# Optimization experiments

Measured on AMD Instinct MI355X. Metric: run time of the kernel, lower is better.

The kernel has to match this reference:

```python
import jax, jax.numpy as jnp
import numpy as np

N_HEAD = 8

def _l2norm(x, eps=1e-12):
    # F.normalize(p=2, dim=-1): x / max(||x||_2, eps)
    return x / jnp.maximum(jnp.linalg.norm(x, axis=-1, keepdims=True), eps)

def setup_inputs() -> dict:
    key = jax.random.key(0)
    ks = jax.random.split(key, 9)
    B, L, E = 2, 2048, 512
    s = 0.02
    return {
        "query": jax.random.normal(ks[0], (B, L, E), dtype=jnp.float32),
        "Wq": s * jax.random.normal(ks[1], (E, E), dtype=jnp.float32),
        "bq": jnp.zeros((E,), dtype=jnp.float32),
        "Wk": s * jax.random.normal(ks[2], (E, E), dtype=jnp.float32),
        "bk": jnp.zeros((E,), dtype=jnp.float32),
        "Wv": s * jax.random.normal(ks[3], (E, E), dtype=jnp.float32),
        "bv": jnp.zeros((E,), dtype=jnp.float32),
        "Wo": s * jax.random.normal(ks[4], (E, E), dtype=jnp.float32),
        "bo": jnp.zeros((E,), dtype=jnp.float32),
    }

def reference(query, Wq, bq, Wk, bk, Wv, bv, Wo, bo):
    B, L, E = query.shape
    H = N_HEAD
    hd = E // H
    # Faithful to torch: .view(tgt_len, bsz, E) is a RESHAPE, not a transpose.
    x = query.reshape(L, B, E)
    q = jax.nn.relu(x @ Wq.T + bq)
    k = jax.nn.relu(x @ Wk.T + bk)
    v = x @ Wv.T + bv
    q = _l2norm(q)
    k = _l2norm(k)
    # (L, B, E) -> (L, B*H, hd) -> (B*H, L, hd)
    q_ = q.reshape(L, B * H, hd).transpose(1, 0, 2)
    k_ = k.reshape(L, B * H, hd).transpose(1, 0, 2)
    v_ = v.reshape(L, B * H, hd).transpose(1, 0, 2)
    # Causal linear attention: cumulative outer-product of k,v then contract with q.
    kv = jnp.einsum('nld,nlm->nldm', k_, v_)      # [B*H, L, hd, hd]
    kv_cum = jnp.cumsum(kv, axis=1)
    out = jnp.einsum('nld,nldm->nlm', q_, kv_cum)  # [B*H, L, hd]
    out = out.transpose(1, 0, 2).reshape(L, B, E)
    out = out @ Wo.T + bo
    return out.reshape(B, L, E)
```

## Files before the change

### kernel.cpp

```cpp
#include <hip/hip_runtime.h>
#include <hip/hip_bf16.h>

typedef __attribute__((ext_vector_type(8))) short short8;
typedef __attribute__((ext_vector_type(4))) float f32x4;
using bf16 = __hip_bfloat16;

__device__ __forceinline__ unsigned short f2bf(float f) {
    unsigned u = __float_as_uint(f);
    u += 0x7fff + ((u >> 16) & 1);
    return (unsigned short)(u >> 16);
}
__device__ __forceinline__ float bf2f(unsigned short s) {
    return __uint_as_float(((unsigned)s) << 16);
}
__device__ __forceinline__ void gl_lds16(const unsigned short* g, unsigned short* l) {
    __builtin_amdgcn_global_load_lds(
        (const __attribute__((address_space(1))) unsigned int*)g,
        (__attribute__((address_space(3))) unsigned int*)l, 16, 0, 0);
}


__global__ __launch_bounds__(256) void pack_kernel(
    const float* __restrict__ X, const float* __restrict__ Wq, const float* __restrict__ Wk,
    const float* __restrict__ Wv, const float* __restrict__ Wo,
    bf16* __restrict__ Xp, bf16* __restrict__ Wqp, bf16* __restrict__ Wkp,
    bf16* __restrict__ Wvp, bf16* __restrict__ Wop, float* __restrict__ ssq)
{
    __shared__ __align__(16) unsigned short sm[4096];
    int id = blockIdx.x;
    int tid = threadIdx.x;
    if (id < 8) {
        int zi = id * 1024 + tid * 4;
        *(float4*)&ssq[zi] = make_float4(0.f, 0.f, 0.f, 0.f);
    }
    const float* src; unsigned short* dst; int g, sc;
    if (id < 512) { src = X; dst = (unsigned short*)Xp; g = id >> 3; sc = id & 7; }
    else {
        int t = id - 512; int wsel = t >> 6; int u = t & 63;
        g = u >> 3; sc = u & 7;
        src = (wsel == 0) ? Wq : ((wsel == 1) ? Wk : ((wsel == 2) ? Wv : Wo));
        dst = (unsigned short*)((wsel == 0) ? Wqp : ((wsel == 1) ? Wkp : ((wsel == 2) ? Wvp : Wop)));
    }
    int r = tid >> 2, kq = tid & 3;
    const float* sp = src + (size_t)(g * 64 + r) * 512 + sc * 64 + kq * 16;
    #pragma unroll
    for (int i = 0; i < 4; ++i) {
        float4 v = *(const float4*)(sp + i * 4);
        int kk = kq * 16 + i * 4;
        int sl = kk >> 3, el = kk & 7;
        ushort4 u4;
        u4.x = f2bf(v.x); u4.y = f2bf(v.y); u4.z = f2bf(v.z); u4.w = f2bf(v.w);
        *(ushort4*)&sm[(sl * 64 + r) * 8 + el] = u4;
    }
    __syncthreads();
    unsigned short* dp = dst + (size_t)g * 32768 + sc * 4096;
    *(uint4*)(dp + tid * 16)     = *(const uint4*)&sm[tid * 16];
    *(uint4*)(dp + tid * 16 + 8) = *(const uint4*)&sm[tid * 16 + 8];
}

__global__ __launch_bounds__(256) void qkv_gemm_kernel(
    const bf16* __restrict__ Xp,
    const bf16* __restrict__ W0p, const bf16* __restrict__ W1p, const bf16* __restrict__ W2p,
    const float* __restrict__ b0, const float* __restrict__ b1, const float* __restrict__ b2,
    bf16* __restrict__ O0, bf16* __restrict__ O1, bf16* __restrict__ O2,
    float* __restrict__ ssq)
{
    __shared__ __align__(16) unsigned short smem[32768];
    const unsigned short* Ag  = (const unsigned short*)Xp;
    const unsigned short* W0g = (const unsigned short*)W0p;
    const unsigned short* W1g = (const unsigned short*)W1p;
    const unsigned short* W2g = (const unsigned short*)W2p;
    int g = blockIdx.x, gy = blockIdx.y;
    int m0 = g * 64, n0 = gy * 64;
    int tid = threadIdx.x;
    int lane = tid & 63;
    int w = tid >> 6;
    int wm = (w >> 1) * 32;
    int wn = (w & 1) * 32;
    int fr = lane & 15, qf = lane >> 4;

    f32x4 zero4 = {0.f, 0.f, 0.f, 0.f};
    f32x4 acc[3][2][2];
    #pragma unroll
    for (int z = 0; z < 3; ++z)
        #pragma unroll
        for (int t = 0; t < 2; ++t)
            #pragma unroll
            for (int u = 0; u < 2; ++u) acc[z][t][u] = zero4;

#define QKV_STAGE(buf, it) do {                                                              \
        unsigned short* bb = smem + (buf) * 16384;                                           \
        int s0_ = (it) * 8 + w * 2;                                                          \
        gl_lds16(Ag  + ((size_t)(g  * 64 + s0_)     * 64 + lane) * 8, bb + (w * 2)     * 512);        \
        gl_lds16(Ag  + ((size_t)(g  * 64 + s0_ + 1) * 64 + lane) * 8, bb + (w * 2 + 1) * 512);        \
        gl_lds16(W0g + ((size_t)(gy * 64 + s0_)     * 64 + lane) * 8, bb + 4096  + (w * 2)     * 512); \
        gl_lds16(W0g + ((size_t)(gy * 64 + s0_ + 1) * 64 + lane) * 8, bb + 4096  + (w * 2 + 1) * 512); \
        gl_lds16(W1g + ((size_t)(gy * 64 + s0_)     * 64 + lane) * 8, bb + 8192  + (w * 2)     * 512); \
        gl_lds16(W1g + ((size_t)(gy * 64 + s0_ + 1) * 64 + lane) * 8, bb + 8192  + (w * 2 + 1) * 512); \
        gl_lds16(W2g + ((size_t)(gy * 64 + s0_)     * 64 + lane) * 8, bb + 12288 + (w * 2)     * 512); \
        gl_lds16(W2g + ((size_t)(gy * 64 + s0_ + 1) * 64 + lane) * 8, bb + 12288 + (w * 2 + 1) * 512); \
    } while (0)

    int cur = 0;
    QKV_STAGE(0, 0);
    __syncthreads();
    for (int it = 0; it < 8; ++it) {
        if (it < 7) QKV_STAGE(cur ^ 1, it + 1);
        const unsigned short* As = smem + cur * 16384;
        #pragma unroll
        for (int kk = 0; kk < 2; ++kk) {
            int ks = (kk * 4 + qf) * 64;
            short8 af[2];
            af[0] = *(const short8*)&As[(ks + wm + fr) * 8];
            af[1] = *(const short8*)&As[(ks + wm + 16 + fr) * 8];
            #pragma unroll
            for (int z = 0; z < 3; ++z) {
                const unsigned short* Bs = As + 4096 + z * 4096;
                short8 bf0 = *(const short8*)&Bs[(ks + wn + fr) * 8];
                short8 bf1 = *(const short8*)&Bs[(ks + wn + 16 + fr) * 8];
                acc[z][0][0] = __builtin_amdgcn_mfma_f32_16x16x32_bf16(af[0], bf0, acc[z][0][0], 0, 0, 0);
                acc[z][0][1] = __builtin_amdgcn_mfma_f32_16x16x32_bf16(af[0], bf1, acc[z][0][1], 0, 0, 0);
                acc[z][1][0] = __builtin_amdgcn_mfma_f32_16x16x32_bf16(af[1], bf0, acc[z][1][0], 0, 0, 0);
                acc[z][1][1] = __builtin_amdgcn_mfma_f32_16x16x32_bf16(af[1], bf1, acc[z][1][1], 0, 0, 0);
            }
        }
        __syncthreads();
        cur ^= 1;
    }
#undef QKV_STAGE

    int rb = qf * 4;
    #pragma unroll
    for (int z = 0; z < 3; ++z) {
        const float* bias = (z == 0) ? b0 : ((z == 1) ? b1 : b2);
        #pragma unroll
        for (int u = 0; u < 2; ++u) {
            float bv = bias[n0 + wn + u * 16 + fr];
            #pragma unroll
            for (int t = 0; t < 2; ++t)
                #pragma unroll
                for (int r = 0; r < 4; ++r) {
                    float v = acc[z][t][u][r] + bv;
                    if (z < 2) v = fmaxf(v, 0.f);
                    acc[z][t][u][r] = v;
                }
        }
    }
    #pragma unroll
    for (int z = 0; z < 2; ++z)
        #pragma unroll
        for (int t = 0; t < 2; ++t)
            #pragma unroll
            for (int r = 0; r < 4; ++r) {
                float s = acc[z][t][0][r] * acc[z][t][0][r] + acc[z][t][1][r] * acc[z][t][1][r];
                #pragma unroll
                for (int off = 1; off < 16; off <<= 1) s += __shfl_xor(s, off, 64);
                if (fr == 0) atomicAdd(&ssq[z * 4096 + m0 + wm + t * 16 + rb + r], s);
            }
    #pragma unroll
    for (int z = 0; z < 3; ++z)
        #pragma unroll
        for (int t = 0; t < 2; ++t)
            #pragma unroll
            for (int u = 0; u < 2; ++u)
                #pragma unroll
                for (int r = 0; r < 4; ++r)
                    smem[z * 4096 + (wm + t * 16 + rb + r) * 64 + wn + u * 16 + fr] = f2bf(acc[z][t][u][r]);
    __syncthreads();
    unsigned short* O0s = (unsigned short*)O0;
    unsigned short* O1s = (unsigned short*)O1;
    unsigned short* O2s = (unsigned short*)O2;
    #pragma unroll
    for (int rep = 0; rep < 6; ++rep) {
        int idx = rep * 256 + tid;
        int z = idx >> 9, rem = idx & 511;
        int row = rem >> 3, col8 = (rem & 7) * 8;
        unsigned short* Oz = (z == 0) ? O0s : ((z == 1) ? O1s : O2s);
        *(uint4*)(Oz + (size_t)(m0 + row) * 512 + n0 + col8) = *(const uint4*)&smem[z * 4096 + row * 64 + col8];
    }
}

__global__ __launch_bounds__(256) void chunk_kv_kernel(
    const bf16* __restrict__ Kb, const bf16* __restrict__ Vb,
    const float* __restrict__ ssq, bf16* __restrict__ ScT, bf16* __restrict__ Vt_g)
{
    int n = blockIdx.x >> 5, c = blockIdx.x & 31;
    int b = n >> 3, h = n & 7;
    __shared__ float Ks[64 * 64];
    __shared__ float Vs[64 * 64];
    const unsigned short* Kg = (const unsigned short*)Kb;
    const unsigned short* Vg = (const unsigned short*)Vb;
    int tid = threadIdx.x;
    int td = tid >> 4, tm = tid & 15;
    int d0 = td * 4, m0 = tm * 4;
    #pragma unroll
    for (int rep = 0; rep < 4; ++rep) {
        int idx = rep * 1024 + tid * 4;
        int j = idx >> 6, d = idx & 63;
        int grow = (c * 64 + j) * 2 + b;
        ushort4 ku = *(const ushort4*)&Kg[(size_t)grow * 512 + h * 64 + d];
        ushort4 vu = *(const ushort4*)&Vg[(size_t)grow * 512 + h * 64 + d];
        float rk = 1.f / fmaxf(sqrtf(ssq[4096 + grow]), 1e-12f);
        *(float4*)&Ks[j * 64 + d] = make_float4(bf2f(ku.x), bf2f(ku.y), bf2f(ku.z), bf2f(ku.w));
        *(float4*)&Vs[j * 64 + d] = make_float4(bf2f(vu.x) * rk, bf2f(vu.y) * rk,
                                                bf2f(vu.z) * rk, bf2f(vu.w) * rk);
    }
    __syncthreads();
    float acc[4][4] = {};
    for (int j = 0; j < 64; ++j) {
        float4 kv = *(const float4*)&Ks[j * 64 + d0];
        float4 vv = *(const float4*)&Vs[j * 64 + m0];
        acc[0][0] += kv.x*vv.x; acc[0][1] += kv.x*vv.y; acc[0][2] += kv.x*vv.z; acc[0][3] += kv.x*vv.w;
        acc[1][0] += kv.y*vv.x; acc[1][1] += kv.y*vv.y; acc[1][2] += kv.y*vv.z; acc[1][3] += kv.y*vv.w;
        acc[2][0] += kv.z*vv.x; acc[2][1] += kv.z*vv.y; acc[2][2] += kv.z*vv.z; acc[2][3] += kv.z*vv.w;
        acc[3][0] += kv.w*vv.x; acc[3][1] += kv.w*vv.y; acc[3][2] += kv.w*vv.z; acc[3][3] += kv.w*vv.w;
    }
    int vm = tid & 63, vj0 = (tid >> 6) * 16;
    unsigned short tmp[16];
    #pragma unroll
    for (int i = 0; i < 16; ++i) tmp[i] = f2bf(Vs[(vj0 + i) * 64 + vm]);
    size_t vtoff = (size_t)n * 131072 + (size_t)vm * 2048 + c * 64 + vj0;
    *(uint4*)((unsigned short*)Vt_g + vtoff)     = *(uint4*)&tmp[0];
    *(uint4*)((unsigned short*)Vt_g + vtoff + 8) = *(uint4*)&tmp[8];

    unsigned short* outp = (unsigned short*)ScT + (size_t)blockIdx.x * 4096;
    #pragma unroll
    for (int j2 = 0; j2 < 4; ++j2) {
        ushort4 o4;
        o4.x = f2bf(acc[0][j2]); o4.y = f2bf(acc[1][j2]);
        o4.z = f2bf(acc[2][j2]); o4.w = f2bf(acc[3][j2]);
        *(ushort4*)&outp[(m0 + j2) * 64 + d0] = o4;
    }
}

__global__ __launch_bounds__(256) void prefix_kernel(const bf16* __restrict__ ScT, bf16* __restrict__ SpT)
{
    int n = blockIdx.x >> 4;
    int idx = ((blockIdx.x & 15) << 8) + threadIdx.x;
    size_t base = (size_t)n * 131072 + idx;
    const unsigned short* sc = (const unsigned short*)ScT;
    unsigned short* sp = (unsigned short*)SpT;
    float run = 0.f;
    #pragma unroll
    for (int c = 0; c < 32; ++c) {
        size_t off = base + (size_t)c * 4096;
        sp[off] = f2bf(run);
        run += bf2f(sc[off]);
    }
}

__global__ __launch_bounds__(256) void attn_kernel(
    const bf16* __restrict__ Qb, const bf16* __restrict__ Kb,
    const bf16* __restrict__ Vt_g, const bf16* __restrict__ SpT_g,
    const float* __restrict__ ssq, bf16* __restrict__ AOb)
{
    int n = blockIdx.x >> 5, c = blockIdx.x & 31;
    int b = n >> 3, h = n & 7;
    __shared__ __align__(16) unsigned short Qs[64 * 72];
    __shared__ __align__(16) unsigned short Ks[64 * 72];
    __shared__ __align__(16) unsigned short Vt[64 * 72];
    __shared__ __align__(16) unsigned short Ps[4 * 16 * 40];
    int tid = threadIdx.x;
    int lane = tid & 63;
    int w = tid >> 6;
    int fr = lane & 15, q = lane >> 4;

    const unsigned short* Qg = (const unsigned short*)Qb;
    const unsigned short* Kg = (const unsigned short*)Kb;
    const unsigned short* Vg = (const unsigned short*)Vt_g;

    #pragma unroll
    for (int rep = 0; rep < 2; ++rep) {
        int idx = rep * 256 + tid;
        int l = idx >> 3, dc = (idx & 7) * 8;
        size_t goff = (size_t)((c * 64 + l) * 2 + b) * 512 + h * 64 + dc;
        *(uint4*)&Qs[l * 72 + dc] = *(const uint4*)(Qg + goff);
        *(uint4*)&Ks[l * 72 + dc] = *(const uint4*)(Kg + goff);
        int m = l, jc = dc;
        *(uint4*)&Vt[m * 72 + jc] =
            *(const uint4*)(Vg + (size_t)n * 131072 + (size_t)m * 2048 + c * 64 + jc);
    }
    __syncthreads();

    short8 qfr[2];
    #pragma unroll
    for (int kh = 0; kh < 2; ++kh)
        qfr[kh] = *(const short8*)&Qs[(w * 16 + fr) * 72 + kh * 32 + q * 8];

    f32x4 zero4 = {0.f, 0.f, 0.f, 0.f};
    f32x4 oacc[4];
    #pragma unroll
    for (int mt = 0; mt < 4; ++mt) oacc[mt] = zero4;

    const unsigned short* spg = (const unsigned short*)SpT_g + (size_t)blockIdx.x * 4096;
    #pragma unroll
    for (int mt = 0; mt < 4; ++mt) {
        #pragma unroll
        for (int kh = 0; kh < 2; ++kh) {
            short8 sf = *(const short8*)&spg[(mt * 16 + fr) * 64 + kh * 32 + q * 8];
            oacc[mt] = __builtin_amdgcn_mfma_f32_16x16x32_bf16(qfr[kh], sf, oacc[mt], 0, 0, 0);
        }
    }

    unsigned short* myPs = &Ps[w * 640];
    int rbase = q * 4;
    int njt = (w >> 1) + 1;
    for (int jt = 0; jt < njt; ++jt) {
        f32x4 pacc[2];
        pacc[0] = zero4; pacc[1] = zero4;
        #pragma unroll
        for (int jt16 = 0; jt16 < 2; ++jt16) {
            #pragma unroll
            for (int kh = 0; kh < 2; ++kh) {
                short8 kf = *(const short8*)&Ks[(jt * 32 + jt16 * 16 + fr) * 72 + kh * 32 + q * 8];
                pacc[jt16] = __builtin_amdgcn_mfma_f32_16x16x32_bf16(qfr[kh], kf, pacc[jt16], 0, 0, 0);
            }
        }
        bool diag = (jt == njt - 1);
        int lloc = w * 16 + rbase;
        #pragma unroll
        for (int jt16 = 0; jt16 < 2; ++jt16)
            #pragma unroll
            for (int r = 0; r < 4; ++r) {
                int jl = jt * 32 + jt16 * 16 + fr;
                float pv = pacc[jt16][r];
                if (diag && jl > lloc + r) pv = 0.f;
                myPs[(rbase + r) * 40 + jt16 * 16 + fr] = f2bf(pv);
            }
        short8 pf = *(const short8*)&myPs[fr * 40 + q * 8];
        #pragma unroll
        for (int mt = 0; mt < 4; ++mt) {
            short8 vf = *(const short8*)&Vt[(mt * 16 + fr) * 72 + jt * 32 + q * 8];
            oacc[mt] = __builtin_amdgcn_mfma_f32_16x16x32_bf16(pf, vf, oacc[mt], 0, 0, 0);
        }
    }

    float rqv[4];
    #pragma unroll
    for (int r = 0; r < 4; ++r) {
        int flat = (c * 64 + w * 16 + rbase + r) * 2 + b;
        rqv[r] = 1.f / fmaxf(sqrtf(ssq[flat]), 1e-12f);
    }
    __syncthreads();
    #pragma unroll
    for (int mt = 0; mt < 4; ++mt)
        #pragma unroll
        for (int r = 0; r < 4; ++r)
            Qs[(w * 16 + rbase + r) * 64 + mt * 16 + fr] = f2bf(oacc[mt][r] * rqv[r]);
    __syncthreads();
    #pragma unroll
    for (int rep = 0; rep < 2; ++rep) {
        int idx8 = rep * 256 + tid;
        int sl = idx8 >> 6, l = idx8 & 63;
        *(uint4*)((unsigned short*)AOb +
                  (size_t)(((c * 2 + b) * 64 + h * 8 + sl) * 64 + l) * 8) =
            *(const uint4*)&Qs[l * 64 + sl * 8];
    }
}

__global__ __launch_bounds__(256) void oproj_kernel(
    const bf16* __restrict__ A, const bf16* __restrict__ Wop,
    const float* __restrict__ bias, float* __restrict__ Out)
{
    __shared__ __align__(16) unsigned short smem[16384];
    const unsigned short* Ag = (const unsigned short*)A;
    const unsigned short* Wg = (const unsigned short*)Wop;
    int gp = blockIdx.x;
    int gy = blockIdx.y;
    int n0 = gy * 64;
    int tid = threadIdx.x;
    int lane = tid & 63;
    int w = tid >> 6;
    int fr = lane & 15, qf = lane >> 4;
    int wm = (w >> 1) * 32;
    int wn = (w & 1) * 32;

    f32x4 zero4 = {0.f, 0.f, 0.f, 0.f};
    f32x4 acc[2][2];
    acc[0][0] = zero4; acc[0][1] = zero4; acc[1][0] = zero4; acc[1][1] = zero4;

#define OPJ_STAGE(buf, it) do {                                                             \
        unsigned short* As_ = smem + (buf) * 8192;                                          \
        unsigned short* Bs_ = As_ + 4096;                                                   \
        int s0_ = (it) * 8;                                                                 \
        gl_lds16(Ag + ((size_t)(gp * 64 + s0_ + w * 2)     * 64 + lane) * 8, As_ + w * 1024);        \
        gl_lds16(Ag + ((size_t)(gp * 64 + s0_ + w * 2 + 1) * 64 + lane) * 8, As_ + w * 1024 + 512);  \
        gl_lds16(Wg + ((size_t)(gy * 64 + s0_ + w * 2)     * 64 + lane) * 8, Bs_ + w * 1024);        \
        gl_lds16(Wg + ((size_t)(gy * 64 + s0_ + w * 2 + 1) * 64 + lane) * 8, Bs_ + w * 1024 + 512);  \
    } while (0)

    int cur = 0;
    OPJ_STAGE(0, 0);
    __syncthreads();
    for (int it = 0; it < 8; ++it) {
        if (it < 7) OPJ_STAGE(cur ^ 1, it + 1);
        const unsigned short* As = smem + cur * 8192;
        const unsigned short* Bs = As + 4096;
        #pragma unroll
        for (int kk = 0; kk < 2; ++kk) {
            short8 af[2], bfx[2];
            #pragma unroll
            for (int t = 0; t < 2; ++t)
                af[t] = *(const short8*)&As[((kk * 4 + qf) * 64 + wm + t * 16 + fr) * 8];
            #pragma unroll
            for (int u = 0; u < 2; ++u)
                bfx[u] = *(const short8*)&Bs[((kk * 4 + qf) * 64 + wn + u * 16 + fr) * 8];
            #pragma unroll
            for (int t = 0; t < 2; ++t)
                #pragma unroll
                for (int u = 0; u < 2; ++u)
                    acc[t][u] = __builtin_amdgcn_mfma_f32_16x16x32_bf16(af[t], bfx[u], acc[t][u], 0, 0, 0);
        }
        __syncthreads();
        cur ^= 1;
    }
#undef OPJ_STAGE

    int rb = qf * 4;
    float* Cf = (float*)smem;
    #pragma unroll
    for (int t = 0; t < 2; ++t)
        #pragma unroll
        for (int u = 0; u < 2; ++u) {
            float bv = bias[n0 + wn + u * 16 + fr];
            #pragma unroll
            for (int r = 0; r < 4; ++r)
                Cf[(wm + t * 16 + rb + r) * 64 + wn + u * 16 + fr] = acc[t][u][r] + bv;
        }
    __syncthreads();
    int cbase = (gp >> 1) * 128, bb = gp & 1;
    #pragma unroll
    for (int rep = 0; rep < 4; ++rep) {
        int idx = rep * 256 + tid;
        int l2 = idx >> 4, c4 = (idx & 15) * 4;
        *(float4*)(Out + (size_t)(cbase + l2 * 2 + bb) * 512 + n0 + c4) = *(const float4*)&Cf[l2 * 64 + c4];
    }
}

extern "C" void kernel_launch(void* const* d_in, const int* in_sizes, int n_in,
                              void* d_out, int out_size, void* d_ws, size_t ws_size,
                              hipStream_t stream)
{
    (void)in_sizes; (void)n_in; (void)out_size; (void)ws_size;
    const float* x  = (const float*)d_in[0];
    const float* Wq = (const float*)d_in[1];
    const float* bq = (const float*)d_in[2];
    const float* Wk = (const float*)d_in[3];
    const float* bk = (const float*)d_in[4];
    const float* Wv = (const float*)d_in[5];
    const float* bv = (const float*)d_in[6];
    const float* Wo = (const float*)d_in[7];
    const float* bo = (const float*)d_in[8];
    float* out = (float*)d_out;

    float* ssq = (float*)d_ws;
    bf16* Xp  = (bf16*)(ssq + 8192);
    bf16* Wqp = Xp + 2097152;
    bf16* Wkp = Wqp + 262144;
    bf16* Wvp = Wkp + 262144;
    bf16* Wop = Wvp + 262144;
    bf16* Qb  = Wop + 262144;
    bf16* Kb  = Qb + 2097152;
    bf16* Vb  = Kb + 2097152;
    bf16* Vt  = Vb + 2097152;
    bf16* AOb = Vt + 2097152;
    bf16* ScT = AOb + 2097152;
    bf16* SpT = ScT + 2097152;

    pack_kernel<<<768, 256, 0, stream>>>(x, Wq, Wk, Wv, Wo, Xp, Wqp, Wkp, Wvp, Wop, ssq);
    qkv_gemm_kernel<<<dim3(64, 8), 256, 0, stream>>>(Xp, Wqp, Wkp, Wvp, bq, bk, bv, Qb, Kb, Vb, ssq);
    chunk_kv_kernel<<<dim3(512), 256, 0, stream>>>(Kb, Vb, ssq, ScT, Vt);
    prefix_kernel<<<dim3(256), 256, 0, stream>>>(ScT, SpT);
    attn_kernel<<<dim3(512), 256, 0, stream>>>(Qb, Kb, Vt, SpT, ssq, AOb);
    oproj_kernel<<<dim3(64, 8), 256, 0, stream>>>(AOb, Wop, bo, out);
}
```

Measured before the change: 118.2 us.

## Fuse fp32-to-bf16 packing into QKV and output-projection GEMM loads

Removes the separate pack kernel. The QKV GEMM and output-projection GEMM now read fp32 inputs and weights directly, convert them to bf16 in registers and write them to LDS, with register prefetch of the next K-slice. The ssq buffer is zeroed with a memset instead of inside the pack kernel. This saves one launch and the round trip of the packed bf16 arrays through global memory. In exchange, the async global-to-LDS double buffering is lost, weights are re-converted redundantly by every block, and fp32 reads move twice the bytes.

```diff
diff --git a/kernel.cpp b/kernel.cpp
--- a/kernel.cpp
+++ b/kernel.cpp
@@ -20,56 +20,14 @@
 }
 
 
-__global__ __launch_bounds__(256) void pack_kernel(
-    const float* __restrict__ X, const float* __restrict__ Wq, const float* __restrict__ Wk,
-    const float* __restrict__ Wv, const float* __restrict__ Wo,
-    bf16* __restrict__ Xp, bf16* __restrict__ Wqp, bf16* __restrict__ Wkp,
-    bf16* __restrict__ Wvp, bf16* __restrict__ Wop, float* __restrict__ ssq)
-{
-    __shared__ __align__(16) unsigned short sm[4096];
-    int id = blockIdx.x;
-    int tid = threadIdx.x;
-    if (id < 8) {
-        int zi = id * 1024 + tid * 4;
-        *(float4*)&ssq[zi] = make_float4(0.f, 0.f, 0.f, 0.f);
-    }
-    const float* src; unsigned short* dst; int g, sc;
-    if (id < 512) { src = X; dst = (unsigned short*)Xp; g = id >> 3; sc = id & 7; }
-    else {
-        int t = id - 512; int wsel = t >> 6; int u = t & 63;
-        g = u >> 3; sc = u & 7;
-        src = (wsel == 0) ? Wq : ((wsel == 1) ? Wk : ((wsel == 2) ? Wv : Wo));
-        dst = (unsigned short*)((wsel == 0) ? Wqp : ((wsel == 1) ? Wkp : ((wsel == 2) ? Wvp : Wop)));
-    }
-    int r = tid >> 2, kq = tid & 3;
-    const float* sp = src + (size_t)(g * 64 + r) * 512 + sc * 64 + kq * 16;
-    #pragma unroll
-    for (int i = 0; i < 4; ++i) {
-        float4 v = *(const float4*)(sp + i * 4);
-        int kk = kq * 16 + i * 4;
-        int sl = kk >> 3, el = kk & 7;
-        ushort4 u4;
-        u4.x = f2bf(v.x); u4.y = f2bf(v.y); u4.z = f2bf(v.z); u4.w = f2bf(v.w);
-        *(ushort4*)&sm[(sl * 64 + r) * 8 + el] = u4;
-    }
-    __syncthreads();
-    unsigned short* dp = dst + (size_t)g * 32768 + sc * 4096;
-    *(uint4*)(dp + tid * 16)     = *(const uint4*)&sm[tid * 16];
-    *(uint4*)(dp + tid * 16 + 8) = *(const uint4*)&sm[tid * 16 + 8];
-}
-
 __global__ __launch_bounds__(256) void qkv_gemm_kernel(
-    const bf16* __restrict__ Xp,
-    const bf16* __restrict__ W0p, const bf16* __restrict__ W1p, const bf16* __restrict__ W2p,
+    const float* __restrict__ X,
+    const float* __restrict__ W0, const float* __restrict__ W1, const float* __restrict__ W2,
     const float* __restrict__ b0, const float* __restrict__ b1, const float* __restrict__ b2,
     bf16* __restrict__ O0, bf16* __restrict__ O1, bf16* __restrict__ O2,
     float* __restrict__ ssq)
 {
-    __shared__ __align__(16) unsigned short smem[32768];
-    const unsigned short* Ag  = (const unsigned short*)Xp;
-    const unsigned short* W0g = (const unsigned short*)W0p;
-    const unsigned short* W1g = (const unsigned short*)W1p;
-    const unsigned short* W2g = (const unsigned short*)W2p;
+    __shared__ __align__(16) unsigned short smem[16384];
     int g = blockIdx.x, gy = blockIdx.y;
     int m0 = g * 64, n0 = gy * 64;
     int tid = threadIdx.x;
@@ -78,6 +36,13 @@
     int wm = (w >> 1) * 32;
     int wn = (w & 1) * 32;
     int fr = lane & 15, qf = lane >> 4;
+    (void)lane;
+
+    int sr = tid >> 2, skq = tid & 3;
+    const float* xrow = X  + (size_t)(m0 + sr) * 512 + skq * 16;
+    const float* w0r  = W0 + (size_t)(n0 + sr) * 512 + skq * 16;
+    const float* w1r  = W1 + (size_t)(n0 + sr) * 512 + skq * 16;
+    const float* w2r  = W2 + (size_t)(n0 + sr) * 512 + skq * 16;
 
     f32x4 zero4 = {0.f, 0.f, 0.f, 0.f};
     f32x4 acc[3][2][2];
@@ -88,46 +53,55 @@
             #pragma unroll
             for (int u = 0; u < 2; ++u) acc[z][t][u] = zero4;
 
-#define QKV_STAGE(buf, it) do {                                                              \
-        unsigned short* bb = smem + (buf) * 16384;                                           \
-        int s0_ = (it) * 8 + w * 2;                                                          \
-        gl_lds16(Ag  + ((size_t)(g  * 64 + s0_)     * 64 + lane) * 8, bb + (w * 2)     * 512);        \
-        gl_lds16(Ag  + ((size_t)(g  * 64 + s0_ + 1) * 64 + lane) * 8, bb + (w * 2 + 1) * 512);        \
-        gl_lds16(W0g + ((size_t)(gy * 64 + s0_)     * 64 + lane) * 8, bb + 4096  + (w * 2)     * 512); \
-        gl_lds16(W0g + ((size_t)(gy * 64 + s0_ + 1) * 64 + lane) * 8, bb + 4096  + (w * 2 + 1) * 512); \
-        gl_lds16(W1g + ((size_t)(gy * 64 + s0_)     * 64 + lane) * 8, bb + 8192  + (w * 2)     * 512); \
-        gl_lds16(W1g + ((size_t)(gy * 64 + s0_ + 1) * 64 + lane) * 8, bb + 8192  + (w * 2 + 1) * 512); \
-        gl_lds16(W2g + ((size_t)(gy * 64 + s0_)     * 64 + lane) * 8, bb + 12288 + (w * 2)     * 512); \
-        gl_lds16(W2g + ((size_t)(gy * 64 + s0_ + 1) * 64 + lane) * 8, bb + 12288 + (w * 2 + 1) * 512); \
+    float4 a4[4], g0[4], g1[4], g2[4];
+#define QKV_LOAD(k0) do {                                           \
+        _Pragma("unroll")                                           \
+        for (int i = 0; i < 4; ++i) {                               \
+            a4[i] = *(const float4*)(xrow + (k0) + i * 4);          \
+            g0[i] = *(const float4*)(w0r  + (k0) + i * 4);          \
+            g1[i] = *(const float4*)(w1r  + (k0) + i * 4);          \
+            g2[i] = *(const float4*)(w2r  + (k0) + i * 4);          \
+        }                                                           \
     } while (0)
 
-    int cur = 0;
-    QKV_STAGE(0, 0);
-    __syncthreads();
+    QKV_LOAD(0);
     for (int it = 0; it < 8; ++it) {
-        if (it < 7) QKV_STAGE(cur ^ 1, it + 1);
-        const unsigned short* As = smem + cur * 16384;
+        __syncthreads();
+        #pragma unroll
+        for (int i = 0; i < 4; ++i) {
+            int kk = skq * 16 + i * 4;
+            int sl = kk >> 3, el = kk & 7;
+            int cell = (sl * 64 + sr) * 8 + el;
+            ushort4 ua, u0, u1, u2;
+            ua.x = f2bf(a4[i].x); ua.y = f2bf(a4[i].y); ua.z = f2bf(a4[i].z); ua.w = f2bf(a4[i].w);
+            u0.x = f2bf(g0[i].x); u0.y = f2bf(g0[i].y); u0.z = f2bf(g0[i].z); u0.w = f2bf(g0[i].w);
+            u1.x = f2bf(g1[i].x); u1.y = f2bf(g1[i].y); u1.z = f2bf(g1[i].z); u1.w = f2bf(g1[i].w);
+            u2.x = f2bf(g2[i].x); u2.y = f2bf(g2[i].y); u2.z = f2bf(g2[i].z); u2.w = f2bf(g2[i].w);
+            *(ushort4*)&smem[cell]         = ua;
+            *(ushort4*)&smem[4096  + cell] = u0;
+            *(ushort4*)&smem[8192  + cell] = u1;
+            *(ushort4*)&smem[12288 + cell] = u2;
+        }
+        if (it < 7) QKV_LOAD((it + 1) * 64);
+        __syncthreads();
         #pragma unroll
         for (int kk = 0; kk < 2; ++kk) {
             int ks = (kk * 4 + qf) * 64;
-            short8 af[2];
-            af[0] = *(const short8*)&As[(ks + wm + fr) * 8];
-            af[1] = *(const short8*)&As[(ks + wm + 16 + fr) * 8];
+            short8 af0 = *(const short8*)&smem[(ks + wm + fr) * 8];
+            short8 af1 = *(const short8*)&smem[(ks + wm + 16 + fr) * 8];
             #pragma unroll
             for (int z = 0; z < 3; ++z) {
-                const unsigned short* Bs = As + 4096 + z * 4096;
+                const unsigned short* Bs = smem + 4096 + z * 4096;
                 short8 bf0 = *(const short8*)&Bs[(ks + wn + fr) * 8];
                 short8 bf1 = *(const short8*)&Bs[(ks + wn + 16 + fr) * 8];
-                acc[z][0][0] = __builtin_amdgcn_mfma_f32_16x16x32_bf16(af[0], bf0, acc[z][0][0], 0, 0, 0);
-                acc[z][0][1] = __builtin_amdgcn_mfma_f32_16x16x32_bf16(af[0], bf1, acc[z][0][1], 0, 0, 0);
-                acc[z][1][0] = __builtin_amdgcn_mfma_f32_16x16x32_bf16(af[1], bf0, acc[z][1][0], 0, 0, 0);
-                acc[z][1][1] = __builtin_amdgcn_mfma_f32_16x16x32_bf16(af[1], bf1, acc[z][1][1], 0, 0, 0);
+                acc[z][0][0] = __builtin_amdgcn_mfma_f32_16x16x32_bf16(af0, bf0, acc[z][0][0], 0, 0, 0);
+                acc[z][0][1] = __builtin_amdgcn_mfma_f32_16x16x32_bf16(af0, bf1, acc[z][0][1], 0, 0, 0);
+                acc[z][1][0] = __builtin_amdgcn_mfma_f32_16x16x32_bf16(af1, bf0, acc[z][1][0], 0, 0, 0);
+                acc[z][1][1] = __builtin_amdgcn_mfma_f32_16x16x32_bf16(af1, bf1, acc[z][1][1], 0, 0, 0);
             }
         }
-        __syncthreads();
-        cur ^= 1;
-    }
-#undef QKV_STAGE
+    }
+#undef QKV_LOAD
 
     int rb = qf * 4;
     #pragma unroll
@@ -157,6 +131,7 @@
                 for (int off = 1; off < 16; off <<= 1) s += __shfl_xor(s, off, 64);
                 if (fr == 0) atomicAdd(&ssq[z * 4096 + m0 + wm + t * 16 + rb + r], s);
             }
+    __syncthreads();
     #pragma unroll
     for (int z = 0; z < 3; ++z)
         #pragma unroll
@@ -359,12 +334,13 @@
 }
 
 __global__ __launch_bounds__(256) void oproj_kernel(
-    const bf16* __restrict__ A, const bf16* __restrict__ Wop,
+    const bf16* __restrict__ A, const float* __restrict__ Wo,
     const float* __restrict__ bias, float* __restrict__ Out)
 {
-    __shared__ __align__(16) unsigned short smem[16384];
+    __shared__ __align__(16) unsigned short smem[8192];
     const unsigned short* Ag = (const unsigned short*)A;
-    const unsigned short* Wg = (const unsigned short*)Wop;
+    unsigned short* As = smem;
+    unsigned short* Bs = smem + 4096;
     int gp = blockIdx.x;
     int gy = blockIdx.y;
     int n0 = gy * 64;
@@ -374,28 +350,28 @@
     int fr = lane & 15, qf = lane >> 4;
     int wm = (w >> 1) * 32;
     int wn = (w & 1) * 32;
+    int sr = tid >> 2, skq = tid & 3;
+    const float* worow = Wo + (size_t)(n0 + sr) * 512 + skq * 16;
 
     f32x4 zero4 = {0.f, 0.f, 0.f, 0.f};
     f32x4 acc[2][2];
     acc[0][0] = zero4; acc[0][1] = zero4; acc[1][0] = zero4; acc[1][1] = zero4;
 
-#define OPJ_STAGE(buf, it) do {                                                             \
-        unsigned short* As_ = smem + (buf) * 8192;                                          \
-        unsigned short* Bs_ = As_ + 4096;                                                   \
-        int s0_ = (it) * 8;                                                                 \
-        gl_lds16(Ag + ((size_t)(gp * 64 + s0_ + w * 2)     * 64 + lane) * 8, As_ + w * 1024);        \
-        gl_lds16(Ag + ((size_t)(gp * 64 + s0_ + w * 2 + 1) * 64 + lane) * 8, As_ + w * 1024 + 512);  \
-        gl_lds16(Wg + ((size_t)(gy * 64 + s0_ + w * 2)     * 64 + lane) * 8, Bs_ + w * 1024);        \
-        gl_lds16(Wg + ((size_t)(gy * 64 + s0_ + w * 2 + 1) * 64 + lane) * 8, Bs_ + w * 1024 + 512);  \
-    } while (0)
-
-    int cur = 0;
-    OPJ_STAGE(0, 0);
-    __syncthreads();
     for (int it = 0; it < 8; ++it) {
-        if (it < 7) OPJ_STAGE(cur ^ 1, it + 1);
-        const unsigned short* As = smem + cur * 8192;
-        const unsigned short* Bs = As + 4096;
+        int s0 = it * 8, k0 = it * 64;
+        __syncthreads();
+        gl_lds16(Ag + ((size_t)(gp * 64 + s0 + w * 2)     * 64 + lane) * 8, As + w * 1024);
+        gl_lds16(Ag + ((size_t)(gp * 64 + s0 + w * 2 + 1) * 64 + lane) * 8, As + w * 1024 + 512);
+        #pragma unroll
+        for (int i = 0; i < 4; ++i) {
+            float4 v = *(const float4*)(worow + k0 + i * 4);
+            int kk = skq * 16 + i * 4;
+            int sl = kk >> 3, el = kk & 7;
+            ushort4 u;
+            u.x = f2bf(v.x); u.y = f2bf(v.y); u.z = f2bf(v.z); u.w = f2bf(v.w);
+            *(ushort4*)&Bs[(sl * 64 + sr) * 8 + el] = u;
+        }
+        __syncthreads();
         #pragma unroll
         for (int kk = 0; kk < 2; ++kk) {
             short8 af[2], bfx[2];
@@ -411,13 +387,11 @@
                 for (int u = 0; u < 2; ++u)
                     acc[t][u] = __builtin_amdgcn_mfma_f32_16x16x32_bf16(af[t], bfx[u], acc[t][u], 0, 0, 0);
         }
-        __syncthreads();
-        cur ^= 1;
-    }
-#undef OPJ_STAGE
+    }
 
     int rb = qf * 4;
     float* Cf = (float*)smem;
+    __syncthreads();
     #pragma unroll
     for (int t = 0; t < 2; ++t)
         #pragma unroll
@@ -454,12 +428,7 @@
     float* out = (float*)d_out;
 
     float* ssq = (float*)d_ws;
-    bf16* Xp  = (bf16*)(ssq + 8192);
-    bf16* Wqp = Xp + 2097152;
-    bf16* Wkp = Wqp + 262144;
-    bf16* Wvp = Wkp + 262144;
-    bf16* Wop = Wvp + 262144;
-    bf16* Qb  = Wop + 262144;
+    bf16* Qb  = (bf16*)(ssq + 8192);
     bf16* Kb  = Qb + 2097152;
     bf16* Vb  = Kb + 2097152;
     bf16* Vt  = Vb + 2097152;
@@ -467,10 +436,10 @@
     bf16* ScT = AOb + 2097152;
     bf16* SpT = ScT + 2097152;
 
-    pack_kernel<<<768, 256, 0, stream>>>(x, Wq, Wk, Wv, Wo, Xp, Wqp, Wkp, Wvp, Wop, ssq);
-    qkv_gemm_kernel<<<dim3(64, 8), 256, 0, stream>>>(Xp, Wqp, Wkp, Wvp, bq, bk, bv, Qb, Kb, Vb, ssq);
+    hipMemsetAsync(ssq, 0, 8192 * sizeof(float), stream);
+    qkv_gemm_kernel<<<dim3(64, 8), 256, 0, stream>>>(x, Wq, Wk, Wv, bq, bk, bv, Qb, Kb, Vb, ssq);
     chunk_kv_kernel<<<dim3(512), 256, 0, stream>>>(Kb, Vb, ssq, ScT, Vt);
     prefix_kernel<<<dim3(256), 256, 0, stream>>>(ScT, SpT);
     attn_kernel<<<dim3(512), 256, 0, stream>>>(Qb, Kb, Vt, SpT, ssq, AOb);
-    oproj_kernel<<<dim3(64, 8), 256, 0, stream>>>(AOb, Wop, bo, out);
-}
+    oproj_kernel<<<dim3(64, 8), 256, 0, stream>>>(AOb, Wo, bo, out);
+}
```

Result: slower. 129.5 us (+9.6%).
